# Optimization experiments

Measured on AMD Instinct MI355X. Metric: run time of the kernel, lower is better.

The kernel has to match this reference:

```python
import jax, jax.numpy as jnp
import numpy as np

BITS = 4
MAXQ = (1 << BITS) - 1      # 15
PACK = 32 // BITS           # 8 values per int32 word
GROUP = 128                 # quantization group size along K


def setup_inputs() -> dict:
    key = jax.random.key(0)
    k0, k1, k2, k3 = jax.random.split(key, 4)
    M, K, N = 4096, 4096, 11008
    G = K // GROUP
    x = jax.random.normal(k0, (M, K), dtype=jnp.float32)
    # packed 4-bit weights: full-range random int32 words (each holds 8 nibbles)
    qweight = jax.random.randint(k1, (K // PACK, N), -(2**31), 2**31 - 1, dtype=jnp.int32)
    # packed zero points: (G, N // PACK) int32 words
    qzeros = jax.random.randint(k2, (G, N // PACK), -(2**31), 2**31 - 1, dtype=jnp.int32)
    # group-wise scales (G, N), small positive values as GPTQ produces
    scales = jax.random.uniform(k3, (G, N), dtype=jnp.float32, minval=1e-3, maxval=1e-2)
    # standard GPTQ grouping: consecutive blocks of GROUP rows share a group
    g_idx = (jnp.arange(K) // GROUP).astype(jnp.int32)
    return {"x": x, "qweight": qweight, "scales": scales, "qzeros": qzeros, "g_idx": g_idx}


def _dequant(qweight, scales, qzeros, g_idx):
    """Unpack int32-packed 4-bit weights and dequantize to float. Returns (K, N)."""
    K = g_idx.shape[0]
    N = qweight.shape[1]
    k = jnp.arange(K)
    # nibble k lives in word k//PACK at bit offset (k%PACK)*BITS
    k_shift = ((k % PACK) * BITS).astype(jnp.int32)
    w = (qweight[k // PACK] >> k_shift[:, None]) & MAXQ              # (K, N) int32 in [0, MAXQ]
    n = jnp.arange(N)
    n_shift = ((n % PACK) * BITS).astype(jnp.int32)
    z = ((qzeros[:, n // PACK] >> n_shift[None, :]) & MAXQ) + 1      # (G, N); kernel adds 1
    return (w - z[g_idx]).astype(scales.dtype) * scales[g_idx]       # (K, N) float


def reference(x, qweight, scales, qzeros, g_idx):
    # C = A @ dequant(B), fp32 accumulation as in the Triton kernel
    W = _dequant(qweight, scales, qzeros, g_idx)
    return jnp.matmul(x, W, preferred_element_type=jnp.float32)
```

## Files before the change

### kernel.cpp

```cpp
#include <hip/hip_runtime.h>
#include <hip/hip_bf16.h>
#include <stdint.h>

typedef __attribute__((ext_vector_type(8))) short short8;
typedef __attribute__((ext_vector_type(4))) float floatx4;

#define BM 128
#define BN 128
#define BK 64
#define NTHREADS 256
#define GROUP_SZ 128

__device__ __forceinline__ uint32_t cvt_pk_bf16(float lo, float hi) {
    uint32_t r;
    asm("v_cvt_pk_bf16_f32 %0, %1, %2" : "=v"(r) : "v"(lo), "v"(hi));
    return r;
}

__device__ __forceinline__ uint32_t swz(uint32_t row, uint32_t byte_in_row) {
    return row * 128u + (byte_in_row ^ ((row & 7u) << 4));
}

__global__ __launch_bounds__(NTHREADS, 2)
void gptq_gemm_kernel(const float* __restrict__ x,
                      const int* __restrict__ qweight,
                      const float* __restrict__ scales,
                      const int* __restrict__ qzeros,
                      float* __restrict__ out,
                      int M, int K, int N) {
    __shared__ char smem[(BM * BK + BN * BK) * 2];
    char* Ald = smem;
    char* Bld = smem + BM * BK * 2;

    const int nbm = M / BM, nbn = N / BN;
    const int nwg = nbm * nbn;
    int bid = blockIdx.x;
    int q = nwg >> 3, r = nwg & 7;
    int xcd = bid & 7, lin = bid >> 3;
    int sid = (xcd < r ? xcd * (q + 1) : r * (q + 1) + (xcd - r) * q) + lin;
    int bm = sid / nbn, bn = sid % nbn;
    const int m0 = bm * BM, n0 = bn * BN;

    const int t = threadIdx.x;
    const int lane = t & 63, wave = t >> 6;

    const int tm = t >> 4;
    const int tk4 = t & 15;
    const int sn = t & 127;
    const int kwh = t >> 7;

    const int gn = n0 + sn;
    const int NT = K / BK;

    float4 av[8];
    uint32_t qw[4];
    float sc, nz;

    auto load_tile = [&](int ts) {
        const int k0 = ts * BK;
        const float* xb = x + (size_t)(m0 + tm) * K + k0 + tk4 * 4;
        #pragma unroll
        for (int i = 0; i < 8; ++i)
            av[i] = *reinterpret_cast<const float4*>(xb + (size_t)i * 16 * K);
        const int g = k0 >> 7;
        sc = scales[(size_t)g * N + gn];
        const uint32_t zw = (uint32_t)qzeros[(size_t)g * (N >> 3) + (gn >> 3)];
        const float z = (float)((zw >> ((gn & 7) * 4)) & 15u) + 1.0f;
        nz = -z * sc;
        const int* qb = qweight + (size_t)((k0 >> 3) + kwh * 4) * N + gn;
        #pragma unroll
        for (int j = 0; j < 4; ++j)
            qw[j] = (uint32_t)qb[(size_t)j * N];
    };

    auto write_tile = [&]() {
        #pragma unroll
        for (int i = 0; i < 8; ++i) {
            uint2 p;
            p.x = cvt_pk_bf16(av[i].x, av[i].y);
            p.y = cvt_pk_bf16(av[i].z, av[i].w);
            *reinterpret_cast<uint2*>(Ald + swz((uint32_t)(i * 16 + tm), (uint32_t)(tk4 * 8))) = p;
        }
        #pragma unroll
        for (int j = 0; j < 4; ++j) {
            const uint32_t w = qw[j];
            float f[8];
            #pragma unroll
            for (int e = 0; e < 8; ++e)
                f[e] = fmaf((float)((w >> (4 * e)) & 15u), sc, nz);
            uint4 p;
            p.x = cvt_pk_bf16(f[0], f[1]);
            p.y = cvt_pk_bf16(f[2], f[3]);
            p.z = cvt_pk_bf16(f[4], f[5]);
            p.w = cvt_pk_bf16(f[6], f[7]);
            *reinterpret_cast<uint4*>(Bld + swz((uint32_t)sn, (uint32_t)((kwh * 4 + j) * 16))) = p;
        }
    };

    floatx4 acc[4][4];
    const floatx4 fzero = {0.f, 0.f, 0.f, 0.f};
    #pragma unroll
    for (int i = 0; i < 4; ++i)
        #pragma unroll
        for (int j = 0; j < 4; ++j)
            acc[i][j] = fzero;

    const int wm = (wave >> 1) * 64, wn = (wave & 1) * 64;
    const int fr = lane & 15;
    const int fkb = ((lane >> 4) * 8) * 2;

    auto compute = [&]() {
        #pragma unroll
        for (int kk = 0; kk < 2; ++kk) {
            short8 af[4], bf[4];
            #pragma unroll
            for (int i = 0; i < 4; ++i)
                af[i] = *reinterpret_cast<const short8*>(
                    Ald + swz((uint32_t)(wm + i * 16 + fr), (uint32_t)(kk * 64 + fkb)));
            #pragma unroll
            for (int i = 0; i < 4; ++i)
                bf[i] = *reinterpret_cast<const short8*>(
                    Bld + swz((uint32_t)(wn + i * 16 + fr), (uint32_t)(kk * 64 + fkb)));
            #pragma unroll
            for (int i = 0; i < 4; ++i)
                #pragma unroll
                for (int j = 0; j < 4; ++j)
                    acc[i][j] = __builtin_amdgcn_mfma_f32_16x16x32_bf16(af[i], bf[j], acc[i][j], 0, 0, 0);
        }
    };

    load_tile(0);
    write_tile();
    __syncthreads();
    for (int ts = 0; ts < NT; ++ts) {
        if (ts + 1 < NT) load_tile(ts + 1);
        compute();
        __syncthreads();
        if (ts + 1 < NT) write_tile();
        __syncthreads();
    }

    const int fq = lane >> 4;
    float* op = out + (size_t)(m0 + wm) * N + n0 + wn;
    #pragma unroll
    for (int i = 0; i < 4; ++i)
        #pragma unroll
        for (int j = 0; j < 4; ++j)
            #pragma unroll
            for (int rr = 0; rr < 4; ++rr)
                op[(size_t)(i * 16 + fq * 4 + rr) * N + j * 16 + fr] = acc[i][j][rr];
}

extern "C" void kernel_launch(void* const* d_in, const int* in_sizes, int n_in,
                              void* d_out, int out_size, void* d_ws, size_t ws_size,
                              hipStream_t stream) {
    const float* x       = (const float*)d_in[0];
    const int*   qweight = (const int*)d_in[1];
    const float* scales  = (const float*)d_in[2];
    const int*   qzeros  = (const int*)d_in[3];

    const int K = in_sizes[4];
    const int M = in_sizes[0] / K;
    const int G = K / GROUP_SZ;
    const int N = in_sizes[2] / G;
    float* out = (float*)d_out;

    const int nwg = (M / BM) * (N / BN);
    hipLaunchKernelGGL(gptq_gemm_kernel, dim3(nwg), dim3(NTHREADS), 0, stream,
                       x, qweight, scales, qzeros, out, M, K, N);
}
```

Baseline: 476.5 us.

## Split into fp16 pre-conversion passes plus a pipelined 256x256 GEMM

Adds a kernel that converts x to fp16 and another that dequantizes the 4-bit weights into fp16 using magic-number bit tricks. The weights are written to a workspace in a pre-tiled layout. A new 8-wave, 256x256-tile GEMM then streams both operands straight into LDS with global_load_lds, double buffers them, and interleaves MFMA quadrants with barriers and s_setprio. The aim is to take the per-tile conversion and dequant work out of the GEMM inner loop and make the matmul compute-bound. The cost is extra workspace memory traffic, two additional kernel launches, and a switch from bf16 to fp16 operands. The old fused kernel is kept as a fallback when the workspace is too small or the shapes do not divide evenly.

```diff
diff --git a/kernel.cpp b/kernel.cpp
--- a/kernel.cpp
+++ b/kernel.cpp
@@ -2,133 +2,314 @@
 #include <hip/hip_bf16.h>
 #include <stdint.h>
 
+typedef _Float16 half8 __attribute__((ext_vector_type(8)));
 typedef __attribute__((ext_vector_type(8))) short short8;
 typedef __attribute__((ext_vector_type(4))) float floatx4;
-
-#define BM 128
-#define BN 128
-#define BK 64
-#define NTHREADS 256
+typedef __attribute__((ext_vector_type(4))) uint32_t uint32x4;
+
 #define GROUP_SZ 128
+
+__device__ __forceinline__ uint32_t cvt_pk_f16(float lo, float hi) {
+    uint32_t r;
+    asm("v_cvt_pkrtz_f16_f32 %0, %1, %2" : "=v"(r) : "v"(lo), "v"(hi));
+    return r;
+}
+__device__ __forceinline__ uint32_t pk_add_f16(uint32_t a, uint32_t b) {
+    uint32_t r;
+    asm("v_pk_add_f16 %0, %1, %2" : "=v"(r) : "v"(a), "v"(b));
+    return r;
+}
+__device__ __forceinline__ uint32_t pk_mul_f16(uint32_t a, uint32_t b) {
+    uint32_t r;
+    asm("v_pk_mul_f16 %0, %1, %2" : "=v"(r) : "v"(a), "v"(b));
+    return r;
+}
+
+__global__ __launch_bounds__(256)
+void convA_kernel(const float* __restrict__ x, uint4* __restrict__ aws, int total8) {
+    int idx = blockIdx.x * 256 + threadIdx.x;
+    if (idx >= total8) return;
+    const float4* xp = reinterpret_cast<const float4*>(x) + (size_t)idx * 2;
+    float4 a = xp[0], b = xp[1];
+    uint4 o;
+    o.x = cvt_pk_f16(a.x, a.y);
+    o.y = cvt_pk_f16(a.z, a.w);
+    o.z = cvt_pk_f16(b.x, b.y);
+    o.w = cvt_pk_f16(b.z, b.w);
+    aws[idx] = o;
+}
+
+__global__ __launch_bounds__(256)
+void deqB_kernel(const int* __restrict__ qw, const float* __restrict__ sc,
+                 const int* __restrict__ qz, char* __restrict__ bws, int K, int N) {
+    const int n = blockIdx.x * 256 + threadIdx.x;
+    const int wk = blockIdx.y;
+    if (n >= N) return;
+    const uint32_t w = (uint32_t)qw[(size_t)wk * N + n];
+    const int g = wk >> 4;
+    const float s = sc[(size_t)g * N + n];
+    const uint32_t zw = (uint32_t)qz[(size_t)g * (N >> 3) + (n >> 3)];
+    const float zf = -(float)(1025u + ((zw >> ((n & 7) * 4)) & 15u));
+    const uint32_t c2 = cvt_pk_f16(zf, zf);
+    const uint32_t s2 = cvt_pk_f16(s, s);
+    uint32_t oo[4];
+    #pragma unroll
+    for (int i = 0; i < 4; ++i) {
+        const uint32_t tt = w >> (8 * i);
+        const uint32_t qi = ((tt & 0xFu) | 0x64006400u) | ((tt << 12) & 0xF0000u);
+        oo[i] = pk_mul_f16(pk_add_f16(qi, c2), s2);
+    }
+    uint4 o; o.x = oo[0]; o.y = oo[1]; o.z = oo[2]; o.w = oo[3];
+    const int NKT = K >> 6;
+    const int nt = n >> 8, h = (n >> 7) & 1, row = n & 127;
+    const int kt = wk >> 3, slot = wk & 7;
+    size_t off = ((((size_t)nt * NKT + kt) * 2 + h) * 8 + slot) * 2048 + (size_t)row * 16;
+    *reinterpret_cast<uint4*>(bws + off) = o;
+}
+
+__global__ __launch_bounds__(512, 2)
+void gemm8_kernel(const char* __restrict__ Aws, const char* __restrict__ Bws,
+                  float* __restrict__ out, int M, int K, int N) {
+    __shared__ char smem[131072];
+
+    const int NT = K >> 6;
+    const int nbm = M >> 8, nbn = N >> 8;
+    const int nwg = nbm * nbn;
+    int bid = blockIdx.x;
+    int q = nwg >> 3, r = nwg & 7;
+    int xcd = bid & 7, lin = bid >> 3;
+    int sid = (xcd < r ? xcd * (q + 1) : r * (q + 1) + (xcd - r) * q) + lin;
+    const int bm = sid / nbn, bn = sid % nbn;
+    const int m0 = bm << 8, n0 = bn << 8;
+
+    const int tid = threadIdx.x;
+    const int lane = tid & 63, w = tid >> 6;
+    const int wm = w >> 2, wn = w & 3;
+    const int fr = lane & 15, hi = lane >> 4;
+    const int r8 = lane >> 3, c8 = lane & 7;
+
+    const size_t K2 = (size_t)K * 2;
+    const char* aSrc[2][2];
+    #pragma unroll
+    for (int h = 0; h < 2; ++h)
+        #pragma unroll
+        for (int i = 0; i < 2; ++i)
+            aSrc[h][i] = Aws + (size_t)(m0 + h * 128 + w * 16 + i * 8 + r8) * K2
+                             + (size_t)((c8 ^ r8) * 16);
+    const char* bSrc = Bws + (size_t)bn * ((size_t)NT * 32768)
+                           + (size_t)w * 2048 + (size_t)lane * 16;
+
+    auto stageA = [&](uint32_t buf, int h, int kt) {
+        #pragma unroll
+        for (int i = 0; i < 2; ++i) {
+            const char* src = aSrc[h][i] + (size_t)kt * 128;
+            char* dst = smem + buf * 65536u + (uint32_t)h * 16384u
+                             + (uint32_t)w * 2048u + (uint32_t)i * 1024u;
+            __builtin_amdgcn_global_load_lds(
+                (const __attribute__((address_space(1))) void*)src,
+                (__attribute__((address_space(3))) void*)dst, 16, 0, 0);
+        }
+    };
+    auto stageB = [&](uint32_t buf, int h, int kt) {
+        #pragma unroll
+        for (int i = 0; i < 2; ++i) {
+            const char* src = bSrc + ((size_t)kt * 2 + h) * 16384 + (size_t)i * 1024;
+            char* dst = smem + buf * 65536u + 32768u + (uint32_t)h * 16384u
+                             + (uint32_t)w * 2048u + (uint32_t)i * 1024u;
+            __builtin_amdgcn_global_load_lds(
+                (const __attribute__((address_space(1))) void*)src,
+                (__attribute__((address_space(3))) void*)dst, 16, 0, 0);
+        }
+    };
+
+    floatx4 acc[8][4];
+    const floatx4 fz = {0.f, 0.f, 0.f, 0.f};
+    #pragma unroll
+    for (int i = 0; i < 8; ++i)
+        #pragma unroll
+        for (int j = 0; j < 4; ++j) acc[i][j] = fz;
+    half8 af[4][2];
+    half8 bf[2][2][2];
+
+#define LOAD_AF(QM) { _Pragma("unroll") for (int fmi = 0; fmi < 4; ++fmi) { \
+    _Pragma("unroll") for (int kk = 0; kk < 2; ++kk) { \
+        uint32_t row = (uint32_t)(wm * 128 + ((QM) * 4 + fmi) * 16 + fr); \
+        uint32_t p = (uint32_t)((kk * 4 + hi) ^ (fr & 7)); \
+        uint32x4 u = *reinterpret_cast<const uint32x4*>(As + row * 128u + p * 16u); \
+        af[fmi][kk] = __builtin_bit_cast(half8, u); } } }
+
+#define LOAD_BF(QN) { _Pragma("unroll") for (int fnj = 0; fnj < 2; ++fnj) { \
+    _Pragma("unroll") for (int kk = 0; kk < 2; ++kk) { \
+        uint32_t nl = (uint32_t)(wn * 64 + ((QN) * 2 + fnj) * 16 + fr); \
+        uint32_t off = (nl >> 7) * 16384u + (uint32_t)(kk * 4 + hi) * 2048u + (nl & 127u) * 16u; \
+        uint32x4 u = *reinterpret_cast<const uint32x4*>(Bs + off); \
+        bf[QN][fnj][kk] = __builtin_bit_cast(half8, u); } } }
+
+#define MM(QM, QN) { _Pragma("unroll") for (int fmi = 0; fmi < 4; ++fmi) \
+    _Pragma("unroll") for (int fnj = 0; fnj < 2; ++fnj) \
+    _Pragma("unroll") for (int kk = 0; kk < 2; ++kk) \
+        acc[(QM) * 4 + fmi][(QN) * 2 + fnj] = __builtin_amdgcn_mfma_f32_16x16x32_f16( \
+            af[fmi][kk], bf[QN][fnj][kk], acc[(QM) * 4 + fmi][(QN) * 2 + fnj], 0, 0, 0); }
+
+#define WAIT_LGKM() asm volatile("s_waitcnt lgkmcnt(0)" ::: "memory"); \
+                    __builtin_amdgcn_sched_barrier(0)
+
+    stageA(0, 0, 0); stageA(0, 1, 0); stageB(0, 0, 0); stageB(0, 1, 0);
+    if (NT > 1) { stageA(1, 0, 1); stageA(1, 1, 1); }
+    asm volatile("s_waitcnt vmcnt(4)" ::: "memory");
+    __builtin_amdgcn_s_barrier();
+
+    for (int t = 0; t < NT; ++t) {
+        const uint32_t c = (uint32_t)(t & 1), nb = c ^ 1u;
+        const char* As = smem + c * 65536u;
+        const char* Bs = As + 32768u;
+        const bool st1 = (t + 1 < NT);
+        LOAD_AF(0); LOAD_BF(0);
+        if (st1) stageB(nb, 0, t + 1);
+        __builtin_amdgcn_s_barrier();
+        WAIT_LGKM();
+        __builtin_amdgcn_s_setprio(1); MM(0, 0); __builtin_amdgcn_s_setprio(0);
+        __builtin_amdgcn_sched_barrier(0);
+        __builtin_amdgcn_s_barrier();
+        LOAD_BF(1);
+        if (st1) stageB(nb, 1, t + 1);
+        __builtin_amdgcn_s_barrier();
+        WAIT_LGKM();
+        __builtin_amdgcn_s_setprio(1); MM(0, 1); __builtin_amdgcn_s_setprio(0);
+        __builtin_amdgcn_sched_barrier(0);
+        __builtin_amdgcn_s_barrier();
+        LOAD_AF(1);
+        __builtin_amdgcn_s_barrier();
+        WAIT_LGKM();
+        __builtin_amdgcn_s_setprio(1); MM(1, 0); __builtin_amdgcn_s_setprio(0);
+        __builtin_amdgcn_sched_barrier(0);
+        __builtin_amdgcn_s_barrier();
+        __builtin_amdgcn_s_barrier();
+        __builtin_amdgcn_s_setprio(1); MM(1, 1); __builtin_amdgcn_s_setprio(0);
+        __builtin_amdgcn_sched_barrier(0);
+        __builtin_amdgcn_s_barrier();
+        if (st1) {
+            if (t + 2 < NT) {
+                stageA(c, 0, t + 2); stageA(c, 1, t + 2);
+                asm volatile("s_waitcnt vmcnt(4)" ::: "memory");
+            } else {
+                asm volatile("s_waitcnt vmcnt(0)" ::: "memory");
+            }
+            __builtin_amdgcn_s_barrier();
+        }
+    }
+#undef LOAD_AF
+#undef LOAD_BF
+#undef MM
+#undef WAIT_LGKM
+
+    float* op = out + (size_t)(m0 + wm * 128) * N + n0 + wn * 64;
+    #pragma unroll
+    for (int fm = 0; fm < 8; ++fm)
+        #pragma unroll
+        for (int fn = 0; fn < 4; ++fn)
+            #pragma unroll
+            for (int rr = 0; rr < 4; ++rr)
+                op[(size_t)(fm * 16 + hi * 4 + rr) * N + fn * 16 + fr] = acc[fm][fn][rr];
+}
 
 __device__ __forceinline__ uint32_t cvt_pk_bf16(float lo, float hi) {
     uint32_t r;
     asm("v_cvt_pk_bf16_f32 %0, %1, %2" : "=v"(r) : "v"(lo), "v"(hi));
     return r;
 }
-
-__device__ __forceinline__ uint32_t swz(uint32_t row, uint32_t byte_in_row) {
+__device__ __forceinline__ uint32_t fswz(uint32_t row, uint32_t byte_in_row) {
     return row * 128u + (byte_in_row ^ ((row & 7u) << 4));
 }
 
-__global__ __launch_bounds__(NTHREADS, 2)
-void gptq_gemm_kernel(const float* __restrict__ x,
-                      const int* __restrict__ qweight,
-                      const float* __restrict__ scales,
-                      const int* __restrict__ qzeros,
-                      float* __restrict__ out,
-                      int M, int K, int N) {
-    __shared__ char smem[(BM * BK + BN * BK) * 2];
+__global__ __launch_bounds__(256, 2)
+void fused128_kernel(const float* __restrict__ x, const int* __restrict__ qweight,
+                     const float* __restrict__ scales, const int* __restrict__ qzeros,
+                     float* __restrict__ out, int M, int K, int N) {
+    __shared__ char smem[32768];
     char* Ald = smem;
-    char* Bld = smem + BM * BK * 2;
-
-    const int nbm = M / BM, nbn = N / BN;
+    char* Bld = smem + 16384;
+    const int nbm = M / 128, nbn = N / 128;
     const int nwg = nbm * nbn;
     int bid = blockIdx.x;
     int q = nwg >> 3, r = nwg & 7;
     int xcd = bid & 7, lin = bid >> 3;
     int sid = (xcd < r ? xcd * (q + 1) : r * (q + 1) + (xcd - r) * q) + lin;
     int bm = sid / nbn, bn = sid % nbn;
-    const int m0 = bm * BM, n0 = bn * BN;
-
+    const int m0 = bm * 128, n0 = bn * 128;
     const int t = threadIdx.x;
     const int lane = t & 63, wave = t >> 6;
-
-    const int tm = t >> 4;
-    const int tk4 = t & 15;
-    const int sn = t & 127;
-    const int kwh = t >> 7;
-
+    const int tm = t >> 4, tk4 = t & 15;
+    const int sn = t & 127, kwh = t >> 7;
     const int gn = n0 + sn;
-    const int NT = K / BK;
-
-    float4 av[8];
-    uint32_t qw[4];
-    float sc, nz;
-
+    const int NT = K / 64;
+    float4 av[8]; uint32_t qw[4]; float sc; uint32_t zw;
+    const float* xp = x + (size_t)(m0 + tm) * K + tk4 * 4;
+    const int* qp = qweight + (size_t)(kwh * 4) * N + gn;
     auto load_tile = [&](int ts) {
-        const int k0 = ts * BK;
-        const float* xb = x + (size_t)(m0 + tm) * K + k0 + tk4 * 4;
+        const int k0 = ts * 64;
         #pragma unroll
         for (int i = 0; i < 8; ++i)
-            av[i] = *reinterpret_cast<const float4*>(xb + (size_t)i * 16 * K);
+            av[i] = *reinterpret_cast<const float4*>(xp + (size_t)i * 16 * K + k0);
         const int g = k0 >> 7;
         sc = scales[(size_t)g * N + gn];
-        const uint32_t zw = (uint32_t)qzeros[(size_t)g * (N >> 3) + (gn >> 3)];
-        const float z = (float)((zw >> ((gn & 7) * 4)) & 15u) + 1.0f;
-        nz = -z * sc;
-        const int* qb = qweight + (size_t)((k0 >> 3) + kwh * 4) * N + gn;
-        #pragma unroll
-        for (int j = 0; j < 4; ++j)
-            qw[j] = (uint32_t)qb[(size_t)j * N];
-    };
-
+        zw = (uint32_t)qzeros[(size_t)g * (N >> 3) + (gn >> 3)];
+        const int* qb = qp + (size_t)(k0 >> 3) * N;
+        #pragma unroll
+        for (int j = 0; j < 4; ++j) qw[j] = (uint32_t)qb[(size_t)j * N];
+    };
+    const int zsh = (gn & 7) * 4;
     auto write_tile = [&]() {
         #pragma unroll
         for (int i = 0; i < 8; ++i) {
             uint2 p;
             p.x = cvt_pk_bf16(av[i].x, av[i].y);
             p.y = cvt_pk_bf16(av[i].z, av[i].w);
-            *reinterpret_cast<uint2*>(Ald + swz((uint32_t)(i * 16 + tm), (uint32_t)(tk4 * 8))) = p;
-        }
+            *reinterpret_cast<uint2*>(Ald + fswz((uint32_t)(i * 16 + tm), (uint32_t)(tk4 * 8))) = p;
+        }
+        const float z = (float)((zw >> zsh) & 15u) + 1.0f;
+        const float nz = -z * sc;
         #pragma unroll
         for (int j = 0; j < 4; ++j) {
-            const uint32_t w = qw[j];
+            const uint32_t wv = qw[j];
             float f[8];
             #pragma unroll
             for (int e = 0; e < 8; ++e)
-                f[e] = fmaf((float)((w >> (4 * e)) & 15u), sc, nz);
+                f[e] = fmaf((float)((wv >> (4 * e)) & 15u), sc, nz);
             uint4 p;
-            p.x = cvt_pk_bf16(f[0], f[1]);
-            p.y = cvt_pk_bf16(f[2], f[3]);
-            p.z = cvt_pk_bf16(f[4], f[5]);
-            p.w = cvt_pk_bf16(f[6], f[7]);
-            *reinterpret_cast<uint4*>(Bld + swz((uint32_t)sn, (uint32_t)((kwh * 4 + j) * 16))) = p;
-        }
-    };
-
+            p.x = cvt_pk_bf16(f[0], f[1]); p.y = cvt_pk_bf16(f[2], f[3]);
+            p.z = cvt_pk_bf16(f[4], f[5]); p.w = cvt_pk_bf16(f[6], f[7]);
+            *reinterpret_cast<uint4*>(Bld + fswz((uint32_t)sn, (uint32_t)((kwh * 4 + j) * 16))) = p;
+        }
+    };
     floatx4 acc[4][4];
-    const floatx4 fzero = {0.f, 0.f, 0.f, 0.f};
+    const floatx4 fz = {0.f, 0.f, 0.f, 0.f};
     #pragma unroll
     for (int i = 0; i < 4; ++i)
         #pragma unroll
-        for (int j = 0; j < 4; ++j)
-            acc[i][j] = fzero;
-
+        for (int j = 0; j < 4; ++j) acc[i][j] = fz;
     const int wm = (wave >> 1) * 64, wn = (wave & 1) * 64;
     const int fr = lane & 15;
     const int fkb = ((lane >> 4) * 8) * 2;
-
     auto compute = [&]() {
         #pragma unroll
         for (int kk = 0; kk < 2; ++kk) {
-            short8 af[4], bf[4];
+            short8 afv[4], bfv[4];
             #pragma unroll
             for (int i = 0; i < 4; ++i)
-                af[i] = *reinterpret_cast<const short8*>(
-                    Ald + swz((uint32_t)(wm + i * 16 + fr), (uint32_t)(kk * 64 + fkb)));
+                afv[i] = *reinterpret_cast<const short8*>(
+                    Ald + fswz((uint32_t)(wm + i * 16 + fr), (uint32_t)(kk * 64 + fkb)));
             #pragma unroll
             for (int i = 0; i < 4; ++i)
-                bf[i] = *reinterpret_cast<const short8*>(
-                    Bld + swz((uint32_t)(wn + i * 16 + fr), (uint32_t)(kk * 64 + fkb)));
+                bfv[i] = *reinterpret_cast<const short8*>(
+                    Bld + fswz((uint32_t)(wn + i * 16 + fr), (uint32_t)(kk * 64 + fkb)));
             #pragma unroll
             for (int i = 0; i < 4; ++i)
                 #pragma unroll
                 for (int j = 0; j < 4; ++j)
-                    acc[i][j] = __builtin_amdgcn_mfma_f32_16x16x32_bf16(af[i], bf[j], acc[i][j], 0, 0, 0);
-        }
-    };
-
+                    acc[i][j] = __builtin_amdgcn_mfma_f32_16x16x32_bf16(afv[i], bfv[j], acc[i][j], 0, 0, 0);
+        }
+    };
     load_tile(0);
     write_tile();
     __syncthreads();
@@ -139,7 +320,6 @@
         if (ts + 1 < NT) write_tile();
         __syncthreads();
     }
-
     const int fq = lane >> 4;
     float* op = out + (size_t)(m0 + wm) * N + n0 + wn;
     #pragma unroll
@@ -165,7 +345,23 @@
     const int N = in_sizes[2] / G;
     float* out = (float*)d_out;
 
-    const int nwg = (M / BM) * (N / BN);
-    hipLaunchKernelGGL(gptq_gemm_kernel, dim3(nwg), dim3(NTHREADS), 0, stream,
-                       x, qweight, scales, qzeros, out, M, K, N);
-}
+    const size_t needA = (size_t)M * K * 2;
+    const size_t needB = (size_t)K * (size_t)N * 2;
+    const bool ok = (ws_size >= needA + needB) && (M % 256 == 0) && (N % 256 == 0)
+                    && (K % 128 == 0) && (N % 8 == 0);
+    if (ok) {
+        char* aws = (char*)d_ws;
+        char* bws = aws + needA;
+        const int total8 = M * (K / 8);
+        hipLaunchKernelGGL(convA_kernel, dim3((total8 + 255) / 256), dim3(256), 0, stream,
+                           x, (uint4*)aws, total8);
+        hipLaunchKernelGGL(deqB_kernel, dim3((N + 255) / 256, K / 8), dim3(256), 0, stream,
+                           qweight, scales, qzeros, bws, K, N);
+        hipLaunchKernelGGL(gemm8_kernel, dim3((M / 256) * (N / 256)), dim3(512), 0, stream,
+                           aws, bws, out, M, K, N);
+    } else {
+        const int nwg = (M / 128) * (N / 128);
+        hipLaunchKernelGGL(fused128_kernel, dim3(nwg), dim3(256), 0, stream,
+                           x, qweight, scales, qzeros, out, M, K, N);
+    }
+}
```

Measured after the change: 412.8 us. 13.4% less time.
